# Optimization experiments

Hardware: AMD Instinct MI355X
Metric: run time of the kernel (lower is better)

Reference implementation:

```python
import jax, jax.numpy as jnp
import numpy as np

B, T, D, Q = 32, 2048, 512, 512


def setup_inputs() -> dict:
    key = jax.random.key(0)
    k0, k1, k2, k3, k4, k5 = jax.random.split(key, 6)
    output_data = jax.random.normal(k0, (B, T, D), dtype=jnp.float32)
    query = jax.random.normal(k1, (B, Q), dtype=jnp.float32)
    # valid lengths in [1, T] so no row is fully masked
    lengths = jax.random.randint(k2, (B,), 1, T + 1).astype(jnp.int32)
    w = jax.random.normal(k3, (D, D), dtype=jnp.float32) * (1.0 / np.sqrt(D))
    u = jax.random.normal(k4, (D, Q), dtype=jnp.float32) * (1.0 / np.sqrt(Q))
    v = jax.random.normal(k5, (D, 1), dtype=jnp.float32)
    return {"output_data": output_data, "query": query, "lengths": lengths,
            "w": w, "u": u, "v": v}


def reference(output_data, query, lengths, w, u, v):
    # raw_score = W @ output + U @ query (broadcast over seq)   [B, T, D]
    raw = jnp.einsum('btd,ed->bte', output_data, w) \
        + jnp.einsum('bq,eq->be', query, u)[:, None, :]
    # score = tanh(raw) @ v                                     [B, T, 1]
    score = jnp.tanh(raw) @ v
    # additive mask: 0 on valid positions, -inf on padding
    valid = jnp.arange(T)[None, :] < lengths[:, None]           # [B, T]
    score = score + jnp.where(valid, 0.0, -jnp.inf)[:, :, None]
    weights = jax.nn.softmax(score, axis=1)                     # [B, T, 1]
    expectation = jnp.sum(weights * output_data, axis=1)        # [B, D]
    # dropout_rate=0.0 -> dropout is identity
    return score, weights, expectation
```

## Files before the change

### kernel.cpp

```cpp
#include <hip/hip_runtime.h>
#include <math.h>


#define TPB 256
constexpr int B = 32, T = 2048, D = 512, Qd = 512;
constexpr int NROW = B * T;
#define NEG_SENTINEL (-1e30f)

typedef __attribute__((ext_vector_type(8))) short bf16x8;
typedef __attribute__((ext_vector_type(4))) float f32x4;

__device__ __forceinline__ void lds_barrier() {
    asm volatile("s_waitcnt lgkmcnt(0)" ::: "memory");
    __builtin_amdgcn_s_barrier();
}

__device__ __forceinline__ unsigned cvtpk(float a, float b) {
    unsigned r;
    asm("v_cvt_pk_bf16_f32 %0, %1, %2" : "=v"(r) : "v"(a), "v"(b));
    return r;
}
__device__ __forceinline__ unsigned packsplit(float f0, float f1, unsigned& lopack) {
    unsigned hp = cvtpk(f0, f1);
    float h0 = __builtin_bit_cast(float, hp << 16);
    float h1 = __builtin_bit_cast(float, hp & 0xFFFF0000u);
    lopack = cvtpk(f0 - h0, f1 - h1);
    return hp;
}
__device__ __forceinline__ void cvt8(const float4 a, const float4 b, uint4& hi, uint4& lo) {
    hi.x = packsplit(a.x, a.y, lo.x);
    hi.y = packsplit(a.z, a.w, lo.y);
    hi.z = packsplit(b.x, b.y, lo.z);
    hi.w = packsplit(b.z, b.w, lo.w);
}
__device__ __forceinline__ float fast_tanh(float x) {
    float a = fabsf(x);
    float e = __expf(-2.f * a);
    float t = (1.f - e) / (1.f + e);
    return copysignf(t, x);
}

__global__ void k_uq(const float* __restrict__ query, const float* __restrict__ u,
                     float* __restrict__ uq) {
    int b = blockIdx.x;
    __shared__ float q_s[Qd];
    for (int i = threadIdx.x; i < Qd; i += TPB) q_s[i] = query[b * Qd + i];
    __syncthreads();
    for (int e = threadIdx.x; e < D; e += TPB) {
        const float4* urow = (const float4*)(u + (size_t)e * Qd);
        float acc = 0.f;
        for (int q4 = 0; q4 < Qd / 4; ++q4) {
            float4 uu = urow[q4];
            float4 qq = *(const float4*)(q_s + q4 * 4);
            acc += uu.x * qq.x + uu.y * qq.y + uu.z * qq.z + uu.w * qq.w;
        }
        uq[b * D + e] = acc;
    }
}

__global__ void k_convW(const float* __restrict__ W,
                        uint4* __restrict__ WhF, uint4* __restrict__ WlF) {
    const int g = blockIdx.x * 256 + threadIdx.x;
    const int e = g >> 6, s = g & 63;
    const float4* src = (const float4*)(W + (size_t)e * D + s * 8);
    float4 a = src[0], bq = src[1];
    uint4 hi, lo;
    cvt8(a, bq, hi, lo);
    const int nt = e >> 7, cb = (e >> 4) & 7, lo16 = e & 15;
    const int kc = s >> 2, hi4 = s & 3;
    const size_t idx = ((size_t)(nt * 16 + kc) * 8 + cb) * 64 + hi4 * 16 + lo16;
    WhF[idx] = hi;
    WlF[idx] = lo;
}

__global__ __launch_bounds__(256, 3) void k_gemm(
    const float* __restrict__ X,
    const uint4* __restrict__ WhF,
    const uint4* __restrict__ WlF,
    const float* __restrict__ v,
    const float* __restrict__ uqg,
    float* __restrict__ partialS)
{
    __shared__ uint4 Ah[2][4 * 128], Al[2][4 * 128];
    __shared__ float scr[2][128];

    const int gidx = blockIdx.x;
    const int logical = (gidx & 7) * 256 + (gidx >> 3);
    const int mt = logical >> 2, nt = logical & 3;
    const int row0 = mt * 128, e0 = nt * 128;
    const int b = row0 >> 11;

    const int tid = threadIdx.x, lane = tid & 63, wid = tid >> 6;
    const int wm = wid >> 1, wn = wid & 1;
    const int lo16 = lane & 15, hi4 = lane >> 4;
    const int arow = tid & 127, akh = tid >> 7;

    const float4* Xg = (const float4*)(X + (size_t)(row0 + arow) * D + akh * 16);
    const uint4* WhB = WhF + ((size_t)nt * 16) * 8 * 64 + (wn * 4) * 64 + lane;
    const uint4* WlB = WlF + ((size_t)nt * 16) * 8 * 64 + (wn * 4) * 64 + lane;

    f32x4 acc[4][4];
#pragma unroll
    for (int i = 0; i < 4; ++i)
#pragma unroll
        for (int j = 0; j < 4; ++j) acc[i][j] = (f32x4){0.f, 0.f, 0.f, 0.f};

    float4 xr[2][4];
#pragma unroll
    for (int i = 0; i < 4; ++i) xr[0][i] = Xg[i];
#pragma unroll
    for (int i = 0; i < 4; ++i) xr[1][i] = Xg[8 + i];
    uint4 bhr[4];
#pragma unroll
    for (int fc = 0; fc < 4; ++fc) bhr[fc] = WhB[fc * 64];
    {
        uint4 hp, lp;
        cvt8(xr[0][0], xr[0][1], hp, lp);
        Ah[0][(akh * 2 + 0) * 128 + arow] = hp;
        Al[0][(akh * 2 + 0) * 128 + arow] = lp;
        cvt8(xr[0][2], xr[0][3], hp, lp);
        Ah[0][(akh * 2 + 1) * 128 + arow] = hp;
        Al[0][(akh * 2 + 1) * 128 + arow] = lp;
    }

#pragma unroll
    for (int kc = 0; kc < 16; ++kc) {
        const int cur = kc & 1, nxt = cur ^ 1;
        lds_barrier();

        uint4 blr[4];
        {
            const uint4* wl = WlB + (size_t)kc * 512;
#pragma unroll
            for (int fc = 0; fc < 4; ++fc) blr[fc] = wl[fc * 64];
        }

        if (kc + 1 < 16) {
            uint4 hp, lp;
            cvt8(xr[nxt][0], xr[nxt][1], hp, lp);
            Ah[nxt][(akh * 2 + 0) * 128 + arow] = hp;
            Al[nxt][(akh * 2 + 0) * 128 + arow] = lp;
            cvt8(xr[nxt][2], xr[nxt][3], hp, lp);
            Ah[nxt][(akh * 2 + 1) * 128 + arow] = hp;
            Al[nxt][(akh * 2 + 1) * 128 + arow] = lp;
        }

        bf16x8 aH[4], aL[4];
#pragma unroll
        for (int fr = 0; fr < 4; ++fr) {
            const int idx = hi4 * 128 + wm * 64 + fr * 16 + lo16;
            aH[fr] = __builtin_bit_cast(bf16x8, Ah[cur][idx]);
            aL[fr] = __builtin_bit_cast(bf16x8, Al[cur][idx]);
        }

        bf16x8 bHc[4];
#pragma unroll
        for (int fc = 0; fc < 4; ++fc) bHc[fc] = __builtin_bit_cast(bf16x8, bhr[fc]);
        if (kc + 1 < 16) {
            const uint4* wh = WhB + (size_t)(kc + 1) * 512;
#pragma unroll
            for (int fc = 0; fc < 4; ++fc) bhr[fc] = wh[fc * 64];
        }

#pragma unroll
        for (int fc = 0; fc < 4; ++fc)
#pragma unroll
            for (int fr = 0; fr < 4; ++fr)
                acc[fr][fc] = __builtin_amdgcn_mfma_f32_16x16x32_bf16(aH[fr], bHc[fc], acc[fr][fc], 0, 0, 0);
#pragma unroll
        for (int fc = 0; fc < 4; ++fc) {
            const bf16x8 bL = __builtin_bit_cast(bf16x8, blr[fc]);
#pragma unroll
            for (int fr = 0; fr < 4; ++fr)
                acc[fr][fc] = __builtin_amdgcn_mfma_f32_16x16x32_bf16(aH[fr], bL, acc[fr][fc], 0, 0, 0);
        }
#pragma unroll
        for (int fc = 0; fc < 4; ++fc)
#pragma unroll
            for (int fr = 0; fr < 4; ++fr)
                acc[fr][fc] = __builtin_amdgcn_mfma_f32_16x16x32_bf16(aL[fr], bHc[fc], acc[fr][fc], 0, 0, 0);

        if (kc + 2 < 16) {
#pragma unroll
            for (int i = 0; i < 4; ++i) xr[cur][i] = Xg[(kc + 2) * 8 + i];
        }
    }

    const int colbase = e0 + wn * 64;
#pragma unroll
    for (int fr = 0; fr < 4; ++fr) {
        float ps[4] = {0.f, 0.f, 0.f, 0.f};
#pragma unroll
        for (int fc = 0; fc < 4; ++fc) {
            const int col = colbase + fc * 16 + lo16;
            const float uqc = uqg[b * D + col];
            const float vc  = v[col];
#pragma unroll
            for (int i = 0; i < 4; ++i)
                ps[i] += fast_tanh(acc[fr][fc][i] + uqc) * vc;
        }
#pragma unroll
        for (int i = 0; i < 4; ++i) {
            float p = ps[i];
#pragma unroll
            for (int off = 8; off >= 1; off >>= 1) p += __shfl_xor(p, off, 16);
            if (lo16 == 0) scr[wn][wm * 64 + fr * 16 + hi4 * 4 + i] = p;
        }
    }
    __syncthreads();
    if (tid < 128)
        partialS[(size_t)nt * NROW + row0 + tid] = scr[0][tid] + scr[1][tid];
}

__global__ void k_csm(const float* __restrict__ partialS,
                      const int* __restrict__ lengths,
                      float* __restrict__ score,
                      float* __restrict__ weights) {
    __shared__ float s_s[T];
    __shared__ float redm[4], reds[4];
    const int b = blockIdx.x;
    const int len = lengths[b];
    const size_t base = (size_t)b * T;

    float m = -INFINITY;
    for (int t = threadIdx.x; t < T; t += TPB) {
        const size_t i = base + t;
        float s = partialS[i] + partialS[NROW + i]
                + partialS[2 * NROW + i] + partialS[3 * NROW + i];
        s = (t < len) ? s : NEG_SENTINEL;
        score[i] = s;
        s_s[t] = s;
        m = fmaxf(m, s);
    }
#pragma unroll
    for (int off = 32; off >= 1; off >>= 1) m = fmaxf(m, __shfl_xor(m, off, 64));
    if ((threadIdx.x & 63) == 0) redm[threadIdx.x >> 6] = m;
    __syncthreads();
    m = fmaxf(fmaxf(redm[0], redm[1]), fmaxf(redm[2], redm[3]));

    float sum = 0.f;
    for (int t = threadIdx.x; t < T; t += TPB) sum += __expf(s_s[t] - m);
#pragma unroll
    for (int off = 32; off >= 1; off >>= 1) sum += __shfl_xor(sum, off, 64);
    if ((threadIdx.x & 63) == 0) reds[threadIdx.x >> 6] = sum;
    __syncthreads();
    const float inv = 1.f / (reds[0] + reds[1] + reds[2] + reds[3]);

    for (int t = threadIdx.x; t < T; t += TPB)
        weights[base + t] = __expf(s_s[t] - m) * inv;
}

__global__ void k_exp_partial(const float* __restrict__ X, const float* __restrict__ wts,
                              float* __restrict__ part) {
    const int b = blockIdx.x >> 4;
    const int c = blockIdx.x & 15;
    const int t0 = c * 128;
    const int d0 = threadIdx.x * 4;
    const float* Xb = X + ((size_t)b * T + t0) * D + d0;
    const float* wb = wts + (size_t)b * T + t0;
    float4 a = {0.f, 0.f, 0.f, 0.f};
    for (int t = 0; t < 128; ++t) {
        const float wgt = wb[t];
        const float4 x = *(const float4*)(Xb + (size_t)t * D);
        a.x += wgt * x.x; a.y += wgt * x.y; a.z += wgt * x.z; a.w += wgt * x.w;
    }
    *(float4*)(part + ((size_t)(b * 16 + c)) * D + d0) = a;
}

__global__ void k_exp_reduce(const float* __restrict__ part, float* __restrict__ out) {
    const int i = blockIdx.x * TPB + threadIdx.x;
    const int b = i >> 9, d = i & 511;
    float a = 0.f;
#pragma unroll
    for (int c = 0; c < 16; ++c) a += part[((size_t)(b * 16 + c)) * D + d];
    out[i] = a;
}

extern "C" void kernel_launch(void* const* d_in, const int* in_sizes, int n_in,
                              void* d_out, int out_size, void* d_ws, size_t ws_size,
                              hipStream_t stream) {
    const float* X      = (const float*)d_in[0];
    const float* query  = (const float*)d_in[1];
    const int*   len    = (const int*)  d_in[2];
    const float* w      = (const float*)d_in[3];
    const float* u      = (const float*)d_in[4];
    const float* v      = (const float*)d_in[5];

    float* out     = (float*)d_out;
    float* score   = out;
    float* weights = out + (size_t)B * T;
    float* expec   = out + (size_t)2 * B * T;

    float* uq       = (float*)d_ws;
    float* partialS = uq + (size_t)B * D;
    uint4* WhF      = (uint4*)(partialS + (size_t)4 * NROW);
    uint4* WlF      = WhF + 32768;
    float* part     = partialS;

    k_uq         <<<B,            TPB, 0, stream>>>(query, u, uq);
    k_convW      <<<128,          TPB, 0, stream>>>(w, WhF, WlF);
    k_gemm       <<<2048,         TPB, 0, stream>>>(X, WhF, WlF, v, uq, partialS);
    k_csm        <<<B,            TPB, 0, stream>>>(partialS, len, score, weights);
    k_exp_partial<<<B * 16,       128, 0, stream>>>(X, weights, part);
    k_exp_reduce <<<B * D / TPB,  TPB, 0, stream>>>(part, expec);
}
```

Measured before the change: 176.9 us.

## Stage A tiles per-wave in LDS to drop block barriers, widen partial scores

The GEMM kernel now has each wave load, split and stage only its own 64 rows of X into a private, padded LDS region. This replaces the block-wide barriers with a wave-local lgkmcnt wait, and X is loaded one k-chunk ahead in registers. The final cross-wave LDS reduction is removed: each wave writes its partial score directly, so partialS grows to 8 slices, which k_csm then sums. The extra register buffering lowers the occupancy target from 3 to 2 blocks per SM, and the two wn waves now both load and convert the same X rows, doubling that work.

```diff
diff --git a/kernel.cpp b/kernel.cpp
--- a/kernel.cpp
+++ b/kernel.cpp
@@ -9,11 +9,6 @@
 
 typedef __attribute__((ext_vector_type(8))) short bf16x8;
 typedef __attribute__((ext_vector_type(4))) float f32x4;
-
-__device__ __forceinline__ void lds_barrier() {
-    asm volatile("s_waitcnt lgkmcnt(0)" ::: "memory");
-    __builtin_amdgcn_s_barrier();
-}
 
 __device__ __forceinline__ unsigned cvtpk(float a, float b) {
     unsigned r;
@@ -73,7 +68,7 @@
     WlF[idx] = lo;
 }
 
-__global__ __launch_bounds__(256, 3) void k_gemm(
+__global__ __launch_bounds__(256, 2) void k_gemm(
     const float* __restrict__ X,
     const uint4* __restrict__ WhF,
     const uint4* __restrict__ WlF,
@@ -81,8 +76,8 @@
     const float* __restrict__ uqg,
     float* __restrict__ partialS)
 {
-    __shared__ uint4 Ah[2][4 * 128], Al[2][4 * 128];
-    __shared__ float scr[2][128];
+    __shared__ uint2 AhS[4][64][10];
+    __shared__ uint2 AlS[4][64][10];
 
     const int gidx = blockIdx.x;
     const int logical = (gidx & 7) * 256 + (gidx >> 3);
@@ -93,9 +88,8 @@
     const int tid = threadIdx.x, lane = tid & 63, wid = tid >> 6;
     const int wm = wid >> 1, wn = wid & 1;
     const int lo16 = lane & 15, hi4 = lane >> 4;
-    const int arow = tid & 127, akh = tid >> 7;
-
-    const float4* Xg = (const float4*)(X + (size_t)(row0 + arow) * D + akh * 16);
+
+    const float* Xq = X + (size_t)(row0 + wm * 64 + (lane >> 3)) * D + (lane & 7) * 4;
     const uint4* WhB = WhF + ((size_t)nt * 16) * 8 * 64 + (wn * 4) * 64 + lane;
     const uint4* WlB = WlF + ((size_t)nt * 16) * 8 * 64 + (wn * 4) * 64 + lane;
 
@@ -105,29 +99,27 @@
 #pragma unroll
         for (int j = 0; j < 4; ++j) acc[i][j] = (f32x4){0.f, 0.f, 0.f, 0.f};
 
-    float4 xr[2][4];
-#pragma unroll
-    for (int i = 0; i < 4; ++i) xr[0][i] = Xg[i];
-#pragma unroll
-    for (int i = 0; i < 4; ++i) xr[1][i] = Xg[8 + i];
+    float4 xq[2][8];
+#pragma unroll
+    for (int fh = 0; fh < 8; ++fh) {
+        const int fr = fh >> 1, h = fh & 1;
+        xq[0][fh] = *(const float4*)(Xq + (size_t)(fr * 16 + h * 8) * D);
+    }
     uint4 bhr[4];
 #pragma unroll
     for (int fc = 0; fc < 4; ++fc) bhr[fc] = WhB[fc * 64];
-    {
-        uint4 hp, lp;
-        cvt8(xr[0][0], xr[0][1], hp, lp);
-        Ah[0][(akh * 2 + 0) * 128 + arow] = hp;
-        Al[0][(akh * 2 + 0) * 128 + arow] = lp;
-        cvt8(xr[0][2], xr[0][3], hp, lp);
-        Ah[0][(akh * 2 + 1) * 128 + arow] = hp;
-        Al[0][(akh * 2 + 1) * 128 + arow] = lp;
-    }
 
 #pragma unroll
     for (int kc = 0; kc < 16; ++kc) {
         const int cur = kc & 1, nxt = cur ^ 1;
-        lds_barrier();
-
+
+        if (kc + 1 < 16) {
+#pragma unroll
+            for (int fh = 0; fh < 8; ++fh) {
+                const int fr = fh >> 1, h = fh & 1;
+                xq[nxt][fh] = *(const float4*)(Xq + (size_t)(fr * 16 + h * 8) * D + (kc + 1) * 32);
+            }
+        }
         uint4 blr[4];
         {
             const uint4* wl = WlB + (size_t)kc * 512;
@@ -135,22 +127,27 @@
             for (int fc = 0; fc < 4; ++fc) blr[fc] = wl[fc * 64];
         }
 
-        if (kc + 1 < 16) {
-            uint4 hp, lp;
-            cvt8(xr[nxt][0], xr[nxt][1], hp, lp);
-            Ah[nxt][(akh * 2 + 0) * 128 + arow] = hp;
-            Al[nxt][(akh * 2 + 0) * 128 + arow] = lp;
-            cvt8(xr[nxt][2], xr[nxt][3], hp, lp);
-            Ah[nxt][(akh * 2 + 1) * 128 + arow] = hp;
-            Al[nxt][(akh * 2 + 1) * 128 + arow] = lp;
-        }
+#pragma unroll
+        for (int fh = 0; fh < 8; ++fh) {
+            const int fr = fh >> 1, h = fh & 1;
+            const float4 q = xq[cur][fh];
+            uint2 hi2, lo2;
+            hi2.x = packsplit(q.x, q.y, lo2.x);
+            hi2.y = packsplit(q.z, q.w, lo2.y);
+            const int rl = fr * 16 + h * 8 + (lane >> 3);
+            AhS[wid][rl][lane & 7] = hi2;
+            AlS[wid][rl][lane & 7] = lo2;
+        }
+        asm volatile("s_waitcnt lgkmcnt(0)" ::: "memory");
+        __builtin_amdgcn_sched_barrier(0);
 
         bf16x8 aH[4], aL[4];
 #pragma unroll
         for (int fr = 0; fr < 4; ++fr) {
-            const int idx = hi4 * 128 + wm * 64 + fr * 16 + lo16;
-            aH[fr] = __builtin_bit_cast(bf16x8, Ah[cur][idx]);
-            aL[fr] = __builtin_bit_cast(bf16x8, Al[cur][idx]);
+            const uint4 hv = *(const uint4*)&AhS[wid][fr * 16 + lo16][hi4 * 2];
+            const uint4 lv = *(const uint4*)&AlS[wid][fr * 16 + lo16][hi4 * 2];
+            aH[fr] = __builtin_bit_cast(bf16x8, hv);
+            aL[fr] = __builtin_bit_cast(bf16x8, lv);
         }
 
         bf16x8 bHc[4];
@@ -179,14 +176,10 @@
 #pragma unroll
             for (int fr = 0; fr < 4; ++fr)
                 acc[fr][fc] = __builtin_amdgcn_mfma_f32_16x16x32_bf16(aL[fr], bHc[fc], acc[fr][fc], 0, 0, 0);
-
-        if (kc + 2 < 16) {
-#pragma unroll
-            for (int i = 0; i < 4; ++i) xr[cur][i] = Xg[(kc + 2) * 8 + i];
-        }
     }
 
     const int colbase = e0 + wn * 64;
+    float* pS = partialS + (size_t)(nt * 2 + wn) * NROW + row0 + wm * 64;
 #pragma unroll
     for (int fr = 0; fr < 4; ++fr) {
         float ps[4] = {0.f, 0.f, 0.f, 0.f};
@@ -204,12 +197,9 @@
             float p = ps[i];
 #pragma unroll
             for (int off = 8; off >= 1; off >>= 1) p += __shfl_xor(p, off, 16);
-            if (lo16 == 0) scr[wn][wm * 64 + fr * 16 + hi4 * 4 + i] = p;
-        }
-    }
-    __syncthreads();
-    if (tid < 128)
-        partialS[(size_t)nt * NROW + row0 + tid] = scr[0][tid] + scr[1][tid];
+            if (lo16 == 0) pS[fr * 16 + hi4 * 4 + i] = p;
+        }
+    }
 }
 
 __global__ void k_csm(const float* __restrict__ partialS,
@@ -225,8 +215,9 @@
     float m = -INFINITY;
     for (int t = threadIdx.x; t < T; t += TPB) {
         const size_t i = base + t;
-        float s = partialS[i] + partialS[NROW + i]
-                + partialS[2 * NROW + i] + partialS[3 * NROW + i];
+        float s = 0.f;
+#pragma unroll
+        for (int sl = 0; sl < 8; ++sl) s += partialS[(size_t)sl * NROW + i];
         s = (t < len) ? s : NEG_SENTINEL;
         score[i] = s;
         s_s[t] = s;
@@ -293,7 +284,7 @@
 
     float* uq       = (float*)d_ws;
     float* partialS = uq + (size_t)B * D;
-    uint4* WhF      = (uint4*)(partialS + (size_t)4 * NROW);
+    uint4* WhF      = (uint4*)(partialS + (size_t)8 * NROW);
     uint4* WlF      = WhF + 32768;
     float* part     = partialS;
 
```

Measured after the change: 181.3 us. 2.5% more time.
